# Kernel tuning notes

Hardware: AMD Instinct MI355X
Metric: run time of the kernel (lower is better)

Reference implementation:

```python
import jax, jax.numpy as jnp
import numpy as np

T, M, D_IN, N = 4096, 512, 11, 51


def setup_inputs() -> dict:
    key = jax.random.key(0)
    ks = jax.random.split(key, 11)
    s = 1.0 / np.sqrt(N)  # torch LSTMCell/Linear default init scale
    return {
        "input": jax.random.normal(ks[0], (T, M, D_IN), dtype=jnp.float32),
        "W_ih1": jax.random.uniform(ks[1], (4 * N, D_IN), jnp.float32, -s, s),
        "W_hh1": jax.random.uniform(ks[2], (4 * N, N), jnp.float32, -s, s),
        "b_ih1": jax.random.uniform(ks[3], (4 * N,), jnp.float32, -s, s),
        "b_hh1": jax.random.uniform(ks[4], (4 * N,), jnp.float32, -s, s),
        "W_ih2": jax.random.uniform(ks[5], (4 * N, N), jnp.float32, -s, s),
        "W_hh2": jax.random.uniform(ks[6], (4 * N, N), jnp.float32, -s, s),
        "b_ih2": jax.random.uniform(ks[7], (4 * N,), jnp.float32, -s, s),
        "b_hh2": jax.random.uniform(ks[8], (4 * N,), jnp.float32, -s, s),
        "W_lin": jax.random.uniform(ks[9], (1, N), jnp.float32, -s, s),
        "b_lin": jax.random.uniform(ks[10], (1,), jnp.float32, -s, s),
        "future": 0,
    }


def _lstm_cell(x, h, c, W_ih, W_hh, b_ih, b_hh):
    # torch gate order: input, forget, cell(g), output
    gates = x @ W_ih.T + b_ih + h @ W_hh.T + b_hh  # [m, 4n]
    i, f, g, o = jnp.split(gates, 4, axis=-1)
    c_new = jax.nn.sigmoid(f) * c + jax.nn.sigmoid(i) * jnp.tanh(g)
    h_new = jax.nn.sigmoid(o) * jnp.tanh(c_new)
    return h_new, c_new


def reference(input, W_ih1, W_hh1, b_ih1, b_hh1, W_ih2, W_hh2, b_ih2, b_hh2,
              W_lin, b_lin, future):
    m = input.shape[1]
    n = W_hh1.shape[1]
    h1 = jnp.zeros((m, n), jnp.float32)
    c1 = jnp.zeros((m, n), jnp.float32)
    h2 = jnp.zeros((m, n), jnp.float32)
    c2 = jnp.zeros((m, n), jnp.float32)

    def step(carry, x_t):
        h1, c1, h2, c2 = carry
        h1, c1 = _lstm_cell(x_t, h1, c1, W_ih1, W_hh1, b_ih1, b_hh1)
        h2, c2 = _lstm_cell(h1, h2, c2, W_ih2, W_hh2, b_ih2, b_hh2)
        out = h2 @ W_lin.T + b_lin  # [m, 1]
        return (h1, c1, h2, c2), out

    _, outs = jax.lax.scan(step, (h1, c1, h2, c2), input)  # [T, m, 1]
    # torch.stack(outputs, 1).squeeze(2) -> [m, T]
    # (future loop is dimensionally invalid in the original for future>0; future=0)
    return outs[:, :, 0].T
```

## Files before the change

kernel.cpp:

```cpp
#include <hip/hip_runtime.h>

#define T_STEPS 4096
#define M_BATCH 512
#define D_INP   11
#define N_HID   51

typedef float v4f __attribute__((ext_vector_type(4)));

__device__ __forceinline__ float sigmoid_fast(float v) {
    return __builtin_amdgcn_rcpf(1.0f + __expf(-v));
}
__device__ __forceinline__ float tanh_fast(float v) {
    return 2.0f * __builtin_amdgcn_rcpf(1.0f + __expf(-2.0f * v)) - 1.0f;
}
__device__ __forceinline__ float RL(float v, int l) {
    return __uint_as_float(__builtin_amdgcn_readlane(__float_as_uint(v), l));
}

__attribute__((amdgpu_waves_per_eu(2, 2)))
__global__ __launch_bounds__(256)
void lstm2_replk(const float* __restrict__ input,
                 const float* __restrict__ W_ih1, const float* __restrict__ W_hh1,
                 const float* __restrict__ b_ih1, const float* __restrict__ b_hh1,
                 const float* __restrict__ W_ih2, const float* __restrict__ W_hh2,
                 const float* __restrict__ b_ih2, const float* __restrict__ b_hh2,
                 const float* __restrict__ W_lin, const float* __restrict__ b_lin,
                 float* __restrict__ out)
{
    const int  tid   = threadIdx.x;
    const int  col   = blockIdx.x;
    const int  wid   = tid >> 6;
    const int  lane  = tid & 63;
    const bool valid = lane < N_HID;
    const int  ln    = valid ? lane : N_HID - 1;

    __shared__ __align__(16) v4f   pl1[2][64];
    __shared__ __align__(16) v4f   pl2[3][64];
    __shared__ __align__(16) float xs[2][64 * 12];
    __shared__ float outbuf[128];

    v4f wv[41];
    v4f b1v = {0.f,0.f,0.f,0.f}, b2v = {0.f,0.f,0.f,0.f};
    float wlin = 0.f;
    const float blin = b_lin[0];
    float c1 = 0.f, h1r = 0.f, c2 = 0.f, h2r = 0.f;

    #pragma unroll
    for (int q = 0; q < 4; ++q) {
        const int r = q * N_HID + ln;
        if (wid <= 2) b1v[q] = b_ih1[r] + b_hh1[r];
        if (wid >= 2) b2v[q] = b_ih2[r] + b_hh2[r];
        if (wid == 0) {
            #pragma unroll
            for (int i = 0; i < 11; ++i) wv[i][q]      = W_ih1[r * D_INP + i];
            #pragma unroll
            for (int i = 0; i < 30; ++i) wv[11 + i][q] = W_hh1[r * N_HID + i];
        } else if (wid == 1) {
            #pragma unroll
            for (int i = 0; i < 21; ++i) wv[i][q]      = W_hh1[r * N_HID + 30 + i];
            #pragma unroll
            for (int j = 0; j < 20; ++j) wv[21 + j][q] = W_ih2[r * N_HID + j];
        } else if (wid == 2) {
            #pragma unroll
            for (int i = 0; i < 31; ++i) wv[i][q]      = W_ih2[r * N_HID + 20 + i];
            #pragma unroll
            for (int j = 0; j < 10; ++j) wv[31 + j][q] = W_hh2[r * N_HID + j];
        } else {
            #pragma unroll
            for (int i = 0; i < 41; ++i) wv[i][q]      = W_hh2[r * N_HID + 10 + i];
        }
    }
    if (wid == 3) wlin = valid ? W_lin[lane] : 0.f;

    auto xload = [&](int c, int e) -> float {
        int s = e / 11, d = e - s * 11;
        int tc = c * 64 + s; if (tc > T_STEPS - 1) tc = T_STEPS - 1;
        return input[((size_t)tc * M_BATCH + col) * D_INP + d];
    };
    auto xput = [&](int buf, int e, float v) {
        int s = e / 11, d = e - s * 11;
        xs[buf][s * 12 + d] = v;
    };

    for (int i = tid; i < 2 * 768; i += 256) (&xs[0][0])[i] = 0.f;
    __syncthreads();
    {
        xput(0, tid, xload(0, tid));
        xput(0, tid + 256, xload(0, tid + 256));
        if (tid < 192) xput(0, tid + 512, xload(0, tid + 512));
    }
    __syncthreads();

    const int xln = (lane < D_INP) ? lane : (D_INP - 1);
    float xv = (wid == 0) ? xs[0][xln] : 0.f;
    float xr0 = 0.f, xr1 = 0.f, xr2 = 0.f;

    #pragma unroll 1
    for (int t = 0; t <= T_STEPS; ++t) {
        if ((t & 63) == 0) {
            const int c = (t >> 6) + 1;
            xr0 = xload(c, tid);
            xr1 = xload(c, tid + 256);
            if (tid < 192) xr2 = xload(c, tid + 512);
        }

        v4f aP = {0.f,0.f,0.f,0.f}, aS = {0.f,0.f,0.f,0.f};
        if (wid == 0) {
            #pragma unroll
            for (int k = 0; k < 11; ++k) aP += wv[k] * RL(xv, k);
            #pragma unroll
            for (int i = 0; i < 30; ++i) aP += wv[11 + i] * RL(h1r, i);
        } else if (wid == 1) {
            #pragma unroll
            for (int i = 0; i < 21; ++i) aP += wv[i] * RL(h1r, 30 + i);
            #pragma unroll
            for (int j = 0; j < 20; ++j) aS += wv[21 + j] * RL(h1r, j);
        } else if (wid == 2) {
            #pragma unroll
            for (int i = 0; i < 31; ++i) aP += wv[i] * RL(h1r, 20 + i);
            #pragma unroll
            for (int j = 0; j < 10; ++j) aP += wv[31 + j] * RL(h2r, j);
        } else {
            #pragma unroll
            for (int i = 0; i < 41; ++i) aP += wv[i] * RL(h2r, 10 + i);
        }

        if (wid == 0)      pl1[0][lane] = aP;
        else if (wid == 1) { pl1[1][lane] = aP; pl2[0][lane] = aS; }
        else if (wid == 2) pl2[1][lane] = aP;
        else               pl2[2][lane] = aP;
        __syncthreads();

        if (wid <= 2) {
            const v4f g1 = pl1[0][lane] + pl1[1][lane] + b1v;
            const float i1 = sigmoid_fast(g1.x), f1 = sigmoid_fast(g1.y);
            const float gg = tanh_fast(g1.z),    o1 = sigmoid_fast(g1.w);
            c1  = f1 * c1 + i1 * gg;
            h1r = o1 * tanh_fast(c1);
        }
        if (wid >= 2 && t >= 1) {
            const v4f g2 = pl2[0][lane] + pl2[1][lane] + pl2[2][lane] + b2v;
            const float i2 = sigmoid_fast(g2.x), f2 = sigmoid_fast(g2.y);
            const float gg = tanh_fast(g2.z),    o2 = sigmoid_fast(g2.w);
            c2  = f2 * c2 + i2 * gg;
            h2r = o2 * tanh_fast(c2);
            if (wid == 3) {
                float part = wlin * h2r;
                #pragma unroll
                for (int off = 32; off > 0; off >>= 1)
                    part += __shfl_down(part, off, 64);
                if (lane == 0) outbuf[(t - 1) & 127] = part + blin;
            }
        }
        if (wid == 1 && (t & 63) == 1 && t >= 65) {
            const int tb = (t - 65) + lane;
            out[(size_t)col * T_STEPS + tb] = outbuf[tb & 127];
        }
        if ((t & 63) == 32) {
            const int buf = ((t >> 6) + 1) & 1;
            xput(buf, tid, xr0);
            xput(buf, tid + 256, xr1);
            if (tid < 192) xput(buf, tid + 512, xr2);
        }
        if (wid == 0) {
            const int tn = t + 1;
            xv = xs[(tn >> 6) & 1][(tn & 63) * 12 + xln];
        }
        __syncthreads();
    }

    if (wid == 1) {
        const int idx = 4032 + lane;
        out[(size_t)col * T_STEPS + idx] = outbuf[idx & 127];
    }
}

extern "C" void kernel_launch(void* const* d_in, const int* in_sizes, int n_in,
                              void* d_out, int out_size, void* d_ws, size_t ws_size,
                              hipStream_t stream) {
    const float* input = (const float*)d_in[0];
    const float* W_ih1 = (const float*)d_in[1];
    const float* W_hh1 = (const float*)d_in[2];
    const float* b_ih1 = (const float*)d_in[3];
    const float* b_hh1 = (const float*)d_in[4];
    const float* W_ih2 = (const float*)d_in[5];
    const float* W_hh2 = (const float*)d_in[6];
    const float* b_ih2 = (const float*)d_in[7];
    const float* b_hh2 = (const float*)d_in[8];
    const float* W_lin = (const float*)d_in[9];
    const float* b_lin = (const float*)d_in[10];
    float* out = (float*)d_out;

    lstm2_replk<<<M_BATCH, 256, 0, stream>>>(
        input, W_ih1, W_hh1, b_ih1, b_hh1,
        W_ih2, W_hh2, b_ih2, b_hh2, W_lin, b_lin, out);
}
```

Before: 5.153 ms.

## Rewrite LSTM recurrence with bf16 MFMA over 16-sequence blocks using split-precision weights

Replaces the per-sequence fp32 readlane/FMA recurrence with a kernel where each block handles 16 batch columns and computes both layer gate matmuls through bf16 16x16x32 MFMA instructions. Weights are split into hi and lo bf16 parts to approximate fp32 precision, while activations are rounded to bf16 and exchanged through shared memory. The output linear layer is folded in as an extra row of the layer-2 weights. This cuts the block count from 512 to 32, trading per-step FMA work for matrix-core throughput, but it leaves most CUs idle and adds bf16 rounding error on the hidden states.

Result: slower. 8.506 ms (+65.1%).

```diff
diff --git a/kernel.cpp b/kernel.cpp
--- a/kernel.cpp
+++ b/kernel.cpp
@@ -5,7 +5,9 @@
 #define D_INP   11
 #define N_HID   51
 
-typedef float v4f __attribute__((ext_vector_type(4)));
+typedef __attribute__((ext_vector_type(8))) short bf16x8;
+typedef __attribute__((ext_vector_type(4))) float f32x4;
+typedef __attribute__((ext_vector_type(4))) short s16x4;
 
 __device__ __forceinline__ float sigmoid_fast(float v) {
     return __builtin_amdgcn_rcpf(1.0f + __expf(-v));
@@ -13,165 +15,286 @@
 __device__ __forceinline__ float tanh_fast(float v) {
     return 2.0f * __builtin_amdgcn_rcpf(1.0f + __expf(-2.0f * v)) - 1.0f;
 }
-__device__ __forceinline__ float RL(float v, int l) {
-    return __uint_as_float(__builtin_amdgcn_readlane(__float_as_uint(v), l));
-}
-
-__attribute__((amdgpu_waves_per_eu(2, 2)))
+__device__ __forceinline__ ushort f2bf(float f) {
+    uint u = __float_as_uint(f);
+    u += 0x7fffu + ((u >> 16) & 1u);
+    return (ushort)(u >> 16);
+}
+__device__ __forceinline__ float bf2f(ushort h) {
+    return __uint_as_float(((uint)h) << 16);
+}
+
+#define MFMA(A,B,C) __builtin_amdgcn_mfma_f32_16x16x32_bf16((A),(B),(C),0,0,0)
+
+__attribute__((amdgpu_waves_per_eu(1, 1)))
 __global__ __launch_bounds__(256)
-void lstm2_replk(const float* __restrict__ input,
-                 const float* __restrict__ W_ih1, const float* __restrict__ W_hh1,
-                 const float* __restrict__ b_ih1, const float* __restrict__ b_hh1,
-                 const float* __restrict__ W_ih2, const float* __restrict__ W_hh2,
-                 const float* __restrict__ b_ih2, const float* __restrict__ b_hh2,
-                 const float* __restrict__ W_lin, const float* __restrict__ b_lin,
-                 float* __restrict__ out)
+void lstm2_mfma(const float* __restrict__ input,
+                const float* __restrict__ W_ih1, const float* __restrict__ W_hh1,
+                const float* __restrict__ b_ih1, const float* __restrict__ b_hh1,
+                const float* __restrict__ W_ih2, const float* __restrict__ W_hh2,
+                const float* __restrict__ b_ih2, const float* __restrict__ b_hh2,
+                const float* __restrict__ W_lin, const float* __restrict__ b_lin,
+                float* __restrict__ out)
 {
-    const int  tid   = threadIdx.x;
-    const int  col   = blockIdx.x;
-    const int  wid   = tid >> 6;
-    const int  lane  = tid & 63;
-    const bool valid = lane < N_HID;
-    const int  ln    = valid ? lane : N_HID - 1;
-
-    __shared__ __align__(16) v4f   pl1[2][64];
-    __shared__ __align__(16) v4f   pl2[3][64];
-    __shared__ __align__(16) float xs[2][64 * 12];
-    __shared__ float outbuf[128];
-
-    v4f wv[41];
-    v4f b1v = {0.f,0.f,0.f,0.f}, b2v = {0.f,0.f,0.f,0.f};
-    float wlin = 0.f;
-    const float blin = b_lin[0];
-    float c1 = 0.f, h1r = 0.f, c2 = 0.f, h2r = 0.f;
-
+    const int tid  = threadIdx.x;
+    const int wid  = tid >> 6;
+    const int lane = tid & 63;
+    const int mr   = lane & 15;
+    const int g    = lane >> 4;
+    const int col0 = blockIdx.x * 16;
+
+    __shared__ __align__(16) ushort l1act[16][72];
+    __shared__ __align__(16) ushort l2act[16][136];
+    __shared__ __align__(16) ushort xck[2][16][16][12];
+    __shared__ __align__(16) float  outb[16][64];
+    __shared__ __align__(16) float  biasL1v[208];
+    __shared__ __align__(16) float  biasL2v[208];
+
+    for (int i = tid; i < 16 * 72;  i += 256) (&l1act[0][0])[i] = 0;
+    for (int i = tid; i < 16 * 136; i += 256) (&l2act[0][0])[i] = 0;
+    for (int i = tid; i < 2 * 16 * 16 * 12; i += 256) (&xck[0][0][0][0])[i] = 0;
+    for (int i = tid; i < 16 * 64;  i += 256) (&outb[0][0])[i] = 0.f;
+    __syncthreads();
+
+    if (tid < 208) {
+        int r = tid; float b1, b2;
+        if (r < 204) { int u = r >> 2, q = r & 3;
+            b1 = b_ih1[q * 51 + u] + b_hh1[q * 51 + u];
+            b2 = b_ih2[q * 51 + u] + b_hh2[q * 51 + u];
+        } else { b1 = 0.f; b2 = (r == 204) ? b_lin[0] : 0.f; }
+        biasL1v[r] = b1; biasL2v[r] = b2;
+    }
+
+    auto stage = [&](int cn) {
+        #pragma unroll
+        for (int i = 0; i < 11; ++i) {
+            int f = i * 256 + tid;
+            int s = f / 176, r2 = f - s * 176;
+            int cc = r2 / 11, d = r2 - cc * 11;
+            int ts = cn * 16 + s; if (ts > T_STEPS - 1) ts = T_STEPS - 1;
+            xck[cn & 1][s][cc][d] =
+                f2bf(input[((size_t)ts * M_BATCH + col0 + cc) * D_INP + d]);
+        }
+    };
+    stage(0);
+
+    auto wgetL1 = [&](int r, int k) -> float {
+        if (r >= 204) return 0.f;
+        int u = r >> 2, q = r & 3;
+        if (k < 12) return (k < 11) ? W_ih1[(q * 51 + u) * 11 + k] : 0.f;
+        int hu = k - 12; return (hu < 51) ? W_hh1[(q * 51 + u) * 51 + hu] : 0.f;
+    };
+    auto wgetL2 = [&](int r, int k) -> float {
+        if (r == 204) return (k >= 51 && k < 102) ? W_lin[k - 51] : 0.f;
+        if (r > 204) return 0.f;
+        int u = r >> 2, q = r & 3;
+        if (k < 51)  return W_ih2[(q * 51 + u) * 51 + k];
+        if (k < 102) return W_hh2[(q * 51 + u) * 51 + (k - 51)];
+        return 0.f;
+    };
+    auto mkfragL1 = [&](int m, int kt, int ver) -> bf16x8 {
+        bf16x8 fr;
+        #pragma unroll
+        for (int j = 0; j < 8; ++j) {
+            int k = 32 * kt + 16 * (j >> 2) + 4 * g + (j & 3);
+            float w = wgetL1(16 * m + mr, k);
+            ushort hi = f2bf(w);
+            fr[j] = (short)((ver == 0) ? hi : f2bf(w - bf2f(hi)));
+        }
+        return fr;
+    };
+    auto mkfragL2 = [&](int m, int kt, int ver) -> bf16x8 {
+        bf16x8 fr;
+        #pragma unroll
+        for (int j = 0; j < 8; ++j) {
+            int k = 32 * kt + 16 * (j >> 2) + 4 * g + (j & 3);
+            float w = wgetL2(16 * m + mr, k);
+            ushort hi = f2bf(w);
+            fr[j] = (short)((ver == 0) ? hi : f2bf(w - bf2f(hi)));
+        }
+        return fr;
+    };
+
+    bf16x8 afr[40];
+    f32x4  acc[9];
+    float  cst[9];
     #pragma unroll
-    for (int q = 0; q < 4; ++q) {
-        const int r = q * N_HID + ln;
-        if (wid <= 2) b1v[q] = b_ih1[r] + b_hh1[r];
-        if (wid >= 2) b2v[q] = b_ih2[r] + b_hh2[r];
-        if (wid == 0) {
-            #pragma unroll
-            for (int i = 0; i < 11; ++i) wv[i][q]      = W_ih1[r * D_INP + i];
-            #pragma unroll
-            for (int i = 0; i < 30; ++i) wv[11 + i][q] = W_hh1[r * N_HID + i];
-        } else if (wid == 1) {
-            #pragma unroll
-            for (int i = 0; i < 21; ++i) wv[i][q]      = W_hh1[r * N_HID + 30 + i];
-            #pragma unroll
-            for (int j = 0; j < 20; ++j) wv[21 + j][q] = W_ih2[r * N_HID + j];
-        } else if (wid == 2) {
-            #pragma unroll
-            for (int i = 0; i < 31; ++i) wv[i][q]      = W_ih2[r * N_HID + 20 + i];
-            #pragma unroll
-            for (int j = 0; j < 10; ++j) wv[31 + j][q] = W_hh2[r * N_HID + j];
-        } else {
-            #pragma unroll
-            for (int i = 0; i < 41; ++i) wv[i][q]      = W_hh2[r * N_HID + 10 + i];
-        }
-    }
-    if (wid == 3) wlin = valid ? W_lin[lane] : 0.f;
-
-    auto xload = [&](int c, int e) -> float {
-        int s = e / 11, d = e - s * 11;
-        int tc = c * 64 + s; if (tc > T_STEPS - 1) tc = T_STEPS - 1;
-        return input[((size_t)tc * M_BATCH + col) * D_INP + d];
-    };
-    auto xput = [&](int buf, int e, float v) {
-        int s = e / 11, d = e - s * 11;
-        xs[buf][s * 12 + d] = v;
-    };
-
-    for (int i = tid; i < 2 * 768; i += 256) (&xs[0][0])[i] = 0.f;
-    __syncthreads();
-    {
-        xput(0, tid, xload(0, tid));
-        xput(0, tid + 256, xload(0, tid + 256));
-        if (tid < 192) xput(0, tid + 512, xload(0, tid + 512));
+    for (int i = 0; i < 9; ++i) cst[i] = 0.f;
+    const int MB = (wid == 2) ? 0 : 5;
+
+    if (wid == 0) {
+        #pragma unroll
+        for (int m = 0; m < 9; ++m)
+            #pragma unroll
+            for (int kt = 0; kt < 2; ++kt)
+                #pragma unroll
+                for (int v = 0; v < 2; ++v)
+                    afr[(m * 2 + kt) * 2 + v] = mkfragL1(m, kt, v);
+    } else if (wid == 1) {
+        #pragma unroll
+        for (int mm = 0; mm < 4; ++mm)
+            #pragma unroll
+            for (int kt = 0; kt < 2; ++kt)
+                #pragma unroll
+                for (int v = 0; v < 2; ++v)
+                    afr[(mm * 2 + kt) * 2 + v] = mkfragL1(9 + mm, kt, v);
+        #pragma unroll
+        for (int mm = 0; mm < 3; ++mm)
+            #pragma unroll
+            for (int kt = 0; kt < 4; ++kt)
+                #pragma unroll
+                for (int v = 0; v < 2; ++v)
+                    afr[16 + (mm * 4 + kt) * 2 + v] = mkfragL2(10 + mm, kt, v);
+    } else {
+        #pragma unroll
+        for (int mm = 0; mm < 5; ++mm)
+            #pragma unroll
+            for (int kt = 0; kt < 4; ++kt)
+                #pragma unroll
+                for (int v = 0; v < 2; ++v)
+                    afr[(mm * 4 + kt) * 2 + v] = mkfragL2(MB + mm, kt, v);
     }
     __syncthreads();
 
-    const int xln = (lane < D_INP) ? lane : (D_INP - 1);
-    float xv = (wid == 0) ? xs[0][xln] : 0.f;
-    float xr0 = 0.f, xr1 = 0.f, xr2 = 0.f;
+    auto lstm = [&](f32x4 gg, float& cs) -> float {
+        float iv = sigmoid_fast(gg.x), fv = sigmoid_fast(gg.y);
+        float gv = tanh_fast(gg.z),    ov = sigmoid_fast(gg.w);
+        cs = fv * cs + iv * gv;
+        return ov * tanh_fast(cs);
+    };
 
     #pragma unroll 1
-    for (int t = 0; t <= T_STEPS; ++t) {
-        if ((t & 63) == 0) {
-            const int c = (t >> 6) + 1;
-            xr0 = xload(c, tid);
-            xr1 = xload(c, tid + 256);
-            if (tid < 192) xr2 = xload(c, tid + 512);
-        }
-
-        v4f aP = {0.f,0.f,0.f,0.f}, aS = {0.f,0.f,0.f,0.f};
+    for (int t = 0; t <= T_STEPS + 1; ++t) {
+        const int xb = (t >> 4) & 1, xs = t & 15;
+
+        auto loadB1 = [&](int kt) -> bf16x8 {
+            int k0 = 32 * kt + 4 * g;
+            const ushort* pa = (k0 < 12) ? &xck[xb][xs][mr][k0] : &l1act[mr][k0 - 12];
+            s16x4 va = *(const s16x4*)pa;
+            s16x4 vb = *(const s16x4*)&l1act[mr][k0 + 4];
+            bf16x8 r;
+            r[0]=va[0]; r[1]=va[1]; r[2]=va[2]; r[3]=va[3];
+            r[4]=vb[0]; r[5]=vb[1]; r[6]=vb[2]; r[7]=vb[3];
+            return r;
+        };
+        auto loadB2 = [&](int kt) -> bf16x8 {
+            int k0 = 32 * kt + 4 * g;
+            s16x4 va = *(const s16x4*)&l2act[mr][k0];
+            s16x4 vb = *(const s16x4*)&l2act[mr][k0 + 16];
+            bf16x8 r;
+            r[0]=va[0]; r[1]=va[1]; r[2]=va[2]; r[3]=va[3];
+            r[4]=vb[0]; r[5]=vb[1]; r[6]=vb[2]; r[7]=vb[3];
+            return r;
+        };
+
         if (wid == 0) {
-            #pragma unroll
-            for (int k = 0; k < 11; ++k) aP += wv[k] * RL(xv, k);
-            #pragma unroll
-            for (int i = 0; i < 30; ++i) aP += wv[11 + i] * RL(h1r, i);
+            bf16x8 b0 = loadB1(0), b1 = loadB1(1);
+            #pragma unroll
+            for (int m = 0; m < 9; ++m) {
+                f32x4 a = {0.f, 0.f, 0.f, 0.f};
+                a = MFMA(afr[(m*2+0)*2+0], b0, a);
+                a = MFMA(afr[(m*2+0)*2+1], b0, a);
+                a = MFMA(afr[(m*2+1)*2+0], b1, a);
+                a = MFMA(afr[(m*2+1)*2+1], b1, a);
+                acc[m] = a;
+            }
         } else if (wid == 1) {
-            #pragma unroll
-            for (int i = 0; i < 21; ++i) aP += wv[i] * RL(h1r, 30 + i);
-            #pragma unroll
-            for (int j = 0; j < 20; ++j) aS += wv[21 + j] * RL(h1r, j);
-        } else if (wid == 2) {
-            #pragma unroll
-            for (int i = 0; i < 31; ++i) aP += wv[i] * RL(h1r, 20 + i);
-            #pragma unroll
-            for (int j = 0; j < 10; ++j) aP += wv[31 + j] * RL(h2r, j);
+            bf16x8 b0 = loadB1(0), b1 = loadB1(1);
+            bf16x8 b2f0 = loadB2(0), b2f1 = loadB2(1), b2f2 = loadB2(2), b2f3 = loadB2(3);
+            #pragma unroll
+            for (int mm = 0; mm < 4; ++mm) {
+                f32x4 a = {0.f, 0.f, 0.f, 0.f};
+                a = MFMA(afr[(mm*2+0)*2+0], b0, a);
+                a = MFMA(afr[(mm*2+0)*2+1], b0, a);
+                a = MFMA(afr[(mm*2+1)*2+0], b1, a);
+                a = MFMA(afr[(mm*2+1)*2+1], b1, a);
+                acc[mm] = a;
+            }
+            #pragma unroll
+            for (int mm = 0; mm < 3; ++mm) {
+                f32x4 a = {0.f, 0.f, 0.f, 0.f};
+                a = MFMA(afr[16+(mm*4+0)*2+0], b2f0, a);
+                a = MFMA(afr[16+(mm*4+0)*2+1], b2f0, a);
+                a = MFMA(afr[16+(mm*4+1)*2+0], b2f1, a);
+                a = MFMA(afr[16+(mm*4+1)*2+1], b2f1, a);
+                a = MFMA(afr[16+(mm*4+2)*2+0], b2f2, a);
+                a = MFMA(afr[16+(mm*4+2)*2+1], b2f2, a);
+                a = MFMA(afr[16+(mm*4+3)*2+0], b2f3, a);
+                a = MFMA(afr[16+(mm*4+3)*2+1], b2f3, a);
+                acc[4 + mm] = a;
+            }
         } else {
-            #pragma unroll
-            for (int i = 0; i < 41; ++i) aP += wv[i] * RL(h2r, 10 + i);
-        }
-
-        if (wid == 0)      pl1[0][lane] = aP;
-        else if (wid == 1) { pl1[1][lane] = aP; pl2[0][lane] = aS; }
-        else if (wid == 2) pl2[1][lane] = aP;
-        else               pl2[2][lane] = aP;
+            bf16x8 b2f0 = loadB2(0), b2f1 = loadB2(1), b2f2 = loadB2(2), b2f3 = loadB2(3);
+            #pragma unroll
+            for (int mm = 0; mm < 5; ++mm) {
+                f32x4 a = {0.f, 0.f, 0.f, 0.f};
+                a = MFMA(afr[(mm*4+0)*2+0], b2f0, a);
+                a = MFMA(afr[(mm*4+0)*2+1], b2f0, a);
+                a = MFMA(afr[(mm*4+1)*2+0], b2f1, a);
+                a = MFMA(afr[(mm*4+1)*2+1], b2f1, a);
+                a = MFMA(afr[(mm*4+2)*2+0], b2f2, a);
+                a = MFMA(afr[(mm*4+2)*2+1], b2f2, a);
+                a = MFMA(afr[(mm*4+3)*2+0], b2f3, a);
+                a = MFMA(afr[(mm*4+3)*2+1], b2f3, a);
+                acc[mm] = a;
+            }
+        }
         __syncthreads();
 
-        if (wid <= 2) {
-            const v4f g1 = pl1[0][lane] + pl1[1][lane] + b1v;
-            const float i1 = sigmoid_fast(g1.x), f1 = sigmoid_fast(g1.y);
-            const float gg = tanh_fast(g1.z),    o1 = sigmoid_fast(g1.w);
-            c1  = f1 * c1 + i1 * gg;
-            h1r = o1 * tanh_fast(c1);
-        }
-        if (wid >= 2 && t >= 1) {
-            const v4f g2 = pl2[0][lane] + pl2[1][lane] + pl2[2][lane] + b2v;
-            const float i2 = sigmoid_fast(g2.x), f2 = sigmoid_fast(g2.y);
-            const float gg = tanh_fast(g2.z),    o2 = sigmoid_fast(g2.w);
-            c2  = f2 * c2 + i2 * gg;
-            h2r = o2 * tanh_fast(c2);
-            if (wid == 3) {
-                float part = wlin * h2r;
-                #pragma unroll
-                for (int off = 32; off > 0; off >>= 1)
-                    part += __shfl_down(part, off, 64);
-                if (lane == 0) outbuf[(t - 1) & 127] = part + blin;
-            }
-        }
-        if (wid == 1 && (t & 63) == 1 && t >= 65) {
-            const int tb = (t - 65) + lane;
-            out[(size_t)col * T_STEPS + tb] = outbuf[tb & 127];
-        }
-        if ((t & 63) == 32) {
-            const int buf = ((t >> 6) + 1) & 1;
-            xput(buf, tid, xr0);
-            xput(buf, tid + 256, xr1);
-            if (tid < 192) xput(buf, tid + 512, xr2);
-        }
         if (wid == 0) {
-            const int tn = t + 1;
-            xv = xs[(tn >> 6) & 1][(tn & 63) * 12 + xln];
-        }
+            #pragma unroll
+            for (int m = 0; m < 9; ++m) {
+                f32x4 gg = acc[m] + *(const f32x4*)&biasL1v[16 * m + 4 * g];
+                float h = lstm(gg, cst[m]);
+                int u = 4 * m + g;
+                ushort hb = f2bf(h);
+                l1act[mr][u] = hb; l2act[mr][u] = hb;
+            }
+        } else if (wid == 1) {
+            #pragma unroll
+            for (int mm = 0; mm < 4; ++mm) {
+                int m = 9 + mm;
+                f32x4 gg = acc[mm] + *(const f32x4*)&biasL1v[16 * m + 4 * g];
+                float h = lstm(gg, cst[mm]);
+                int u = 4 * m + g;
+                if (u < N_HID) { ushort hb = f2bf(h); l1act[mr][u] = hb; l2act[mr][u] = hb; }
+            }
+            #pragma unroll
+            for (int mm = 0; mm < 3; ++mm) {
+                int m = 10 + mm;
+                f32x4 gg = acc[4 + mm] + *(const f32x4*)&biasL2v[16 * m + 4 * g];
+                if (mm == 2 && g == 3) {
+                    if (t >= 2) outb[mr][(t - 2) & 63] = gg.x;
+                } else if (t >= 1) {
+                    float h = lstm(gg, cst[4 + mm]);
+                    l2act[mr][N_HID + 4 * m + g] = f2bf(h);
+                }
+            }
+        } else {
+            if (t >= 1) {
+                #pragma unroll
+                for (int mm = 0; mm < 5; ++mm) {
+                    int m = MB + mm;
+                    f32x4 gg = acc[mm] + *(const f32x4*)&biasL2v[16 * m + 4 * g];
+                    float h = lstm(gg, cst[mm]);
+                    l2act[mr][N_HID + 4 * m + g] = f2bf(h);
+                }
+            }
+        }
+
+        if ((t & 31) == 2 && t >= 34) {
+            int tb0 = t - 34, cc = tid >> 4, j0 = (tid & 15) * 2;
+            float2 v = *(const float2*)&outb[cc][(tb0 & 63) + j0];
+            *(float2*)&out[(size_t)(col0 + cc) * T_STEPS + tb0 + j0] = v;
+        }
+        if ((t & 15) == 1 && t <= 4081) stage((t >> 4) + 1);
         __syncthreads();
     }
 
-    if (wid == 1) {
-        const int idx = 4032 + lane;
-        out[(size_t)col * T_STEPS + idx] = outbuf[idx & 127];
+    {
+        int tb0 = 4064, cc = tid >> 4, j0 = (tid & 15) * 2;
+        float2 v = *(const float2*)&outb[cc][(tb0 & 63) + j0];
+        *(float2*)&out[(size_t)(col0 + cc) * T_STEPS + tb0 + j0] = v;
     }
 }
 
@@ -191,7 +314,7 @@
     const float* b_lin = (const float*)d_in[10];
     float* out = (float*)d_out;
 
-    lstm2_replk<<<M_BATCH, 256, 0, stream>>>(
+    lstm2_mfma<<<M_BATCH / 16, 256, 0, stream>>>(
         input, W_ih1, W_hh1, b_ih1, b_hh1,
         W_ih2, W_hh2, b_ih2, b_hh2, W_lin, b_lin, out);
 }
```
